# Performance work log

Measured on AMD Instinct MI355X. Metric: run time of the kernel, lower is better.

The kernel has to match this reference:

```python
import jax, jax.numpy as jnp
import numpy as np

NUM_EMBEDDINGS = 1024
EMBEDDING_DIM = 256


def setup_inputs() -> dict:
    key = jax.random.key(0)
    k1, k2 = jax.random.split(key)
    x = jax.random.normal(k1, (64, EMBEDDING_DIM, 32, 32), dtype=jnp.float32)
    # torch.nn.init.uniform_ default is U[0,1)
    embeddings = jax.random.uniform(k2, (EMBEDDING_DIM, NUM_EMBEDDINGS), dtype=jnp.float32)
    return {"x": x, "embeddings": embeddings}


def reference(x, embeddings):
    # x: [B, C, H, W] with C == embedding_dim; embeddings: [D, K]
    B, C, H, W = x.shape
    x_perm = jnp.transpose(x, (0, 2, 3, 1))           # [B, H, W, D]
    flat = x_perm.reshape(-1, C)                      # [N, D]
    sim = flat @ embeddings                           # [N, K] GEMM
    dists = (jnp.sum(flat * flat, axis=1, keepdims=True)
             + jnp.sum(embeddings * embeddings, axis=0)
             - 2.0 * sim)                             # [N, K]
    indices = jnp.argmin(dists, axis=1)               # [N]
    # one-hot @ embeddings.T is just a row gather of embeddings.T
    quantized = embeddings.T[indices]                 # [N, D]
    quantized = quantized.reshape(x_perm.shape)       # [B, H, W, D]
    # straight-through estimator
    q_ste = x_perm + jax.lax.stop_gradient(quantized - x_perm)
    q_ste = jnp.transpose(q_ste, (0, 3, 1, 2))        # [B, C, H, W]
    quantized = jnp.transpose(quantized, (0, 3, 1, 2))
    return q_ste, quantized, indices
```

## Files before the change

### kernel.cpp

```cpp
#include <hip/hip_runtime.h>

typedef unsigned short u16;
typedef unsigned int   u32;

#define DCH  256
#define KCB  1024
#define HW   1024
#define NPOS 65536
#define MARGIN 0.12f

#define ESQ_WS   0
#define IDX_WS   4096
#define FCNT_WS  266240
#define FLIST_WS 266304
#define ESQD_WS  528448ull
#define XH_WS    1048576ull
#define EH_WS    34603008ull

using f32x4 = __attribute__((ext_vector_type(4))) float;
using f16x8 = __attribute__((ext_vector_type(8))) _Float16;

__device__ __forceinline__ u16 f2h(float x) {
    _Float16 h = (_Float16)x;
    return *reinterpret_cast<u16*>(&h);
}
__device__ __forceinline__ u32 umin2(u32 a, u32 b) { return a < b ? a : b; }
__device__ __forceinline__ u32 umax2(u32 a, u32 b) { return a > b ? a : b; }

__device__ __forceinline__ void gl_lds16(const void* g, void* l) {
    __builtin_amdgcn_global_load_lds(
        (const __attribute__((address_space(1))) void*)g,
        (__attribute__((address_space(3))) void*)l, 16, 0, 0);
}

__device__ __forceinline__ void transpose_slice(const float* __restrict__ src,
                                                u16* __restrict__ dst,
                                                int b, int pc, int cc, int tid) {
    __shared__ float Xs[32][260];
    const int p0 = pc * 256;
    const int c0 = cc * 32;
    const size_t nbase = (size_t)b * 1024 + p0;
#pragma unroll
    for (int r = 0; r < 8; ++r) {
        int id4 = tid + 256 * r;
        int c = id4 >> 6;
        int q = id4 & 63;
        float4 v = *reinterpret_cast<const float4*>(
            src + (size_t)b * 262144 + (size_t)(c0 + c) * 1024 + p0 + q * 4);
        *reinterpret_cast<float4*>(&Xs[c][q * 4]) = v;
    }
    __syncthreads();
    const int p = tid;
#pragma unroll
    for (int dg = 0; dg < 4; ++dg) {
        u32 w0, w1, w2, w3;
        {
            float f0 = Xs[dg * 8 + 0][p], f1 = Xs[dg * 8 + 1][p];
            float f2 = Xs[dg * 8 + 2][p], f3 = Xs[dg * 8 + 3][p];
            float f4 = Xs[dg * 8 + 4][p], f5 = Xs[dg * 8 + 5][p];
            float f6 = Xs[dg * 8 + 6][p], f7 = Xs[dg * 8 + 7][p];
            w0 = (u32)f2h(f0) | ((u32)f2h(f1) << 16);
            w1 = (u32)f2h(f2) | ((u32)f2h(f3) << 16);
            w2 = (u32)f2h(f4) | ((u32)f2h(f5) << 16);
            w3 = (u32)f2h(f6) | ((u32)f2h(f7) << 16);
        }
        uint4 ov = {w0, w1, w2, w3};
        *reinterpret_cast<uint4*>(dst + (nbase + p) * 256 + c0 + dg * 8) = ov;
    }
}

__global__ __launch_bounds__(256) void prep_all(const float* __restrict__ X,
                                                const float* __restrict__ E,
                                                u16* __restrict__ Xh,
                                                u16* __restrict__ Eh,
                                                float* __restrict__ esq,
                                                double* __restrict__ esqd,
                                                int* __restrict__ fcnt) {
    const int tid = threadIdx.x;
    const int bid = blockIdx.x;
    if (bid < 2048) {
        transpose_slice(X, Xh, bid >> 5, (bid >> 3) & 3, bid & 7, tid);
    } else if (bid < 2080) {
        int b2 = bid - 2048;
        transpose_slice(E, Eh, 0, (b2 >> 3) & 3, b2 & 7, tid);
    } else {
        if (bid == 2080 && tid == 0) *fcnt = 0;
        int k = (bid - 2080) * 256 + tid;
        double s = 0.0;
#pragma unroll 8
        for (int c = 0; c < DCH; ++c) {
            double e = (double)E[c * KCB + k];
            s = fma(e, e, s);
        }
        esq[k] = (float)s;
        esqd[k] = s;
    }
}

#define BUFS  32768
#define EB_O  16384
#define ESQ_O 65536
#define MRG_O 69632
#define SM_SZ 72704

__global__ __launch_bounds__(256, 2) void vq_main_mfma(
        const u16* __restrict__ XhG, const u16* __restrict__ EhG,
        const float* __restrict__ esq,
        int* __restrict__ idx_out, int* __restrict__ flag_cnt,
        int* __restrict__ flag_list) {
    __shared__ alignas(16) char sm[SM_SZ];
    const int tid = threadIdx.x;
    const int l = tid & 63;
    const int w = tid >> 6;
    const int wm = w >> 1, wn = w & 1;
    const int pbase = blockIdx.x * 128;

    *reinterpret_cast<float4*>(sm + ESQ_O + tid * 16) =
        *reinterpret_cast<const float4*>(esq + tid * 4);

    const int srow = w * 32 + (l >> 3);
    const int sswz = ((l & 7) ^ (l >> 3)) * 16;
    const char* XhB = reinterpret_cast<const char*>(XhG);
    const char* EhB = reinterpret_cast<const char*>(EhG);
    const size_t xbase = (size_t)(pbase + srow) * 512 + sswz;
    const size_t ebase = (size_t)srow * 512 + sswz;

    const int sA0 = (((l >> 4) ^ (l & 7))) * 16;
    const int addrA0 = wm * 8192 + (l & 15) * 128 + sA0;
    const int addrB0 = wn * 8192 + (l & 15) * 128 + sA0;

    auto STAGE = [&](int bufo, int nt, int kt) {
        const size_t xo = xbase + (size_t)kt * 128;
        const size_t eo = ebase + (size_t)nt * 65536 + (size_t)kt * 128;
#pragma unroll
        for (int k = 0; k < 4; ++k) {
            gl_lds16(XhB + xo + k * 4096, sm + bufo + (w * 4 + k) * 1024);
            gl_lds16(EhB + eo + k * 4096, sm + bufo + EB_O + (w * 4 + k) * 1024);
        }
    };

    u32 b1[16], b2[16];
#pragma unroll
    for (int q = 0; q < 16; ++q) { b1[q] = 0xFFFFFFFFu; b2[q] = 0xFFFFFFFFu; }

    STAGE(0, 0, 0);
    __syncthreads();

    int step = 0;
    for (int nt = 0; nt < 8; ++nt) {
        f32x4 acc[4][4];
#pragma unroll
        for (int i = 0; i < 4; ++i)
#pragma unroll
            for (int j = 0; j < 4; ++j)
#pragma unroll
                for (int r = 0; r < 4; ++r) acc[i][j][r] = 0.f;

        for (int kt = 0; kt < 4; ++kt) {
            int nxt = step + 1;
            if (nxt < 32) STAGE((nxt & 1) * BUFS, nxt >> 2, nxt & 3);
            const char* bo = sm + (step & 1) * BUFS;
#pragma unroll
            for (int ds = 0; ds < 2; ++ds) {
                const int so = ds * 64;
                f16x8 a[4], bh[4];
#pragma unroll
                for (int i = 0; i < 4; ++i)
                    a[i] = *reinterpret_cast<const f16x8*>(bo + ((addrA0 ^ so) + i * 2048));
#pragma unroll
                for (int j = 0; j < 4; ++j)
                    bh[j] = *reinterpret_cast<const f16x8*>(bo + EB_O + ((addrB0 ^ so) + j * 2048));
#pragma unroll
                for (int i = 0; i < 4; ++i)
#pragma unroll
                    for (int j = 0; j < 4; ++j)
                        acc[i][j] = __builtin_amdgcn_mfma_f32_16x16x32_f16(a[i], bh[j], acc[i][j], 0, 0, 0);
            }
            __syncthreads();
            ++step;
        }

        const int kb = nt * 128 + wn * 64 + (l & 15);
        float eq[4];
#pragma unroll
        for (int j = 0; j < 4; ++j)
            eq[j] = *reinterpret_cast<const float*>(sm + ESQ_O + (kb + j * 16) * 4);
#pragma unroll
        for (int i = 0; i < 4; ++i)
#pragma unroll
            for (int j = 0; j < 4; ++j)
#pragma unroll
                for (int r = 0; r < 4; ++r) {
                    float s = fmaxf(fmaf(-2.f, acc[i][j][r], eq[j]), 0.f);
                    u32 v = (__float_as_uint(s) & 0xFFFFFC00u) | (u32)(kb + j * 16);
                    int ri = i * 4 + r;
                    u32 m1 = umin2(b1[ri], v);
                    b2[ri] = umin2(b2[ri], umax2(b1[ri], v));
                    b1[ri] = m1;
                }
    }

#pragma unroll
    for (int m = 1; m <= 8; m <<= 1) {
#pragma unroll
        for (int q = 0; q < 16; ++q) {
            u32 ob1 = (u32)__shfl_xor((int)b1[q], m);
            u32 ob2 = (u32)__shfl_xor((int)b2[q], m);
            u32 mx = umax2(b1[q], ob1);
            b1[q] = umin2(b1[q], ob1);
            b2[q] = umin2(umin2(b2[q], ob2), mx);
        }
    }

    if ((l & 15) == 0) {
#pragma unroll
        for (int i = 0; i < 4; ++i)
#pragma unroll
            for (int r = 0; r < 4; ++r) {
                int q = i * 4 + r;
                int rl = wm * 64 + i * 16 + (l >> 4) * 4 + r;
                *reinterpret_cast<u32*>(sm + MRG_O + (rl * 2 + wn) * 4) = b1[q];
                *reinterpret_cast<u32*>(sm + MRG_O + 1024 + (rl * 2 + wn) * 4) = b2[q];
            }
    }
    __syncthreads();
    if (tid < 128) {
        u32 a1 = *reinterpret_cast<u32*>(sm + MRG_O + (tid * 2 + 0) * 4);
        u32 a2 = *reinterpret_cast<u32*>(sm + MRG_O + 1024 + (tid * 2 + 0) * 4);
        u32 c1 = *reinterpret_cast<u32*>(sm + MRG_O + (tid * 2 + 1) * 4);
        u32 c2 = *reinterpret_cast<u32*>(sm + MRG_O + 1024 + (tid * 2 + 1) * 4);
        u32 P1 = umin2(a1, c1);
        u32 P2 = umin2(umin2(a2, c2), umax2(a1, c1));
        int n = pbase + tid;
        idx_out[n] = (int)(P1 & 1023u);
        float f1 = __uint_as_float(P1 & 0xFFFFFC00u);
        float f2 = __uint_as_float(P2 & 0xFFFFFC00u);
        if (f2 - f1 < MARGIN) {
            int s2 = atomicAdd(flag_cnt, 1);
            flag_list[s2] = n;
        }
    }
}

#define RFPB 4
__global__ __launch_bounds__(256) void vq_repair(const float* __restrict__ X,
                                                 const float* __restrict__ E,
                                                 const double* __restrict__ esqd,
                                                 int* __restrict__ idx_out,
                                                 const int* __restrict__ flag_cnt,
                                                 const int* __restrict__ flag_list) {
    __shared__ double xs[RFPB][256];
    __shared__ double rd[RFPB][256];
    __shared__ int    ri[RFPB][256];
    const int tid = threadIdx.x;
    const int cnt = *flag_cnt;
    for (int f0 = blockIdx.x * RFPB; f0 < cnt; f0 += gridDim.x * RFPB) {
#pragma unroll
        for (int g = 0; g < RFPB; ++g) {
            int f = f0 + g;
            int n = flag_list[f < cnt ? f : f0];
            int b = n >> 10, p = n & 1023;
            xs[g][tid] = (double)X[(size_t)b * 262144 + (size_t)tid * 1024 + p];
        }
        __syncthreads();
        double s[RFPB][4];
#pragma unroll
        for (int g = 0; g < RFPB; ++g)
#pragma unroll
            for (int j = 0; j < 4; ++j) s[g][j] = 0.0;
        const float4* Erow = reinterpret_cast<const float4*>(E) + tid;
#pragma unroll 2
        for (int c = 0; c < 256; ++c) {
            float4 ev = Erow[c * 256];
            double e0 = (double)ev.x, e1 = (double)ev.y, e2 = (double)ev.z, e3 = (double)ev.w;
#pragma unroll
            for (int g = 0; g < RFPB; ++g) {
                double xv = xs[g][c];
                s[g][0] = fma(xv, e0, s[g][0]);
                s[g][1] = fma(xv, e1, s[g][1]);
                s[g][2] = fma(xv, e2, s[g][2]);
                s[g][3] = fma(xv, e3, s[g][3]);
            }
        }
        const int k0 = tid * 4;
        const double eq0 = esqd[k0], eq1 = esqd[k0 + 1], eq2 = esqd[k0 + 2], eq3 = esqd[k0 + 3];
#pragma unroll
        for (int g = 0; g < RFPB; ++g) {
            double d0 = eq0 - 2.0 * s[g][0];
            double d1 = eq1 - 2.0 * s[g][1];
            double d2 = eq2 - 2.0 * s[g][2];
            double d3 = eq3 - 2.0 * s[g][3];
            double bd = d0; int bi = k0;
            if (d1 < bd) { bd = d1; bi = k0 + 1; }
            if (d2 < bd) { bd = d2; bi = k0 + 2; }
            if (d3 < bd) { bd = d3; bi = k0 + 3; }
            rd[g][tid] = bd; ri[g][tid] = bi;
        }
        __syncthreads();
        for (int off = 128; off > 0; off >>= 1) {
            if (tid < off) {
#pragma unroll
                for (int g = 0; g < RFPB; ++g) {
                    double od = rd[g][tid + off]; int oi = ri[g][tid + off];
                    if (od < rd[g][tid] || (od == rd[g][tid] && oi < ri[g][tid])) {
                        rd[g][tid] = od; ri[g][tid] = oi;
                    }
                }
            }
            __syncthreads();
        }
        if (tid < RFPB && (f0 + tid) < cnt) {
            idx_out[flag_list[f0 + tid]] = ri[tid][0];
        }
        __syncthreads();
    }
}

#define WCC 8
__global__ __launch_bounds__(256) void vq_write(const float* __restrict__ E,
                                                const int* __restrict__ idx_ws,
                                                float* __restrict__ out0,
                                                float* __restrict__ out1,
                                                float* __restrict__ out2) {
    __shared__ float Es[WCC][1024];
    const int tid = threadIdx.x;
    const int b   = blockIdx.x >> 5;
    const int cch = blockIdx.x & 31;
#pragma unroll
    for (int r = 0; r < 8; ++r) {
        int id4 = tid + 256 * r;
        int c = id4 >> 8;
        int q = id4 & 255;
        *reinterpret_cast<float4*>(&Es[c][q * 4]) =
            *reinterpret_cast<const float4*>(E + (size_t)(cch * WCC + c) * 1024 + q * 4);
    }
    int4 kv = *reinterpret_cast<const int4*>(idx_ws + b * 1024 + tid * 4);
    __syncthreads();
    if (cch == 0) {
        float4 v = {(float)kv.x, (float)kv.y, (float)kv.z, (float)kv.w};
        *reinterpret_cast<float4*>(out2 + b * 1024 + tid * 4) = v;
    }
#pragma unroll
    for (int c = 0; c < WCC; ++c) {
        float4 v = {Es[c][kv.x], Es[c][kv.y], Es[c][kv.z], Es[c][kv.w]};
        size_t o = (size_t)b * 262144 + (size_t)(cch * WCC + c) * 1024 + tid * 4;
        *reinterpret_cast<float4*>(out0 + o) = v;
        *reinterpret_cast<float4*>(out1 + o) = v;
    }
}

extern "C" void kernel_launch(void* const* d_in, const int* in_sizes, int n_in,
                              void* d_out, int out_size, void* d_ws, size_t ws_size,
                              hipStream_t stream) {
    const float* X = (const float*)d_in[0];
    const float* E = (const float*)d_in[1];
    float* out = (float*)d_out;
    char* ws = (char*)d_ws;

    float* esq   = (float*)(ws + ESQ_WS);
    int* idx     = (int*)(ws + IDX_WS);
    int* fcnt    = (int*)(ws + FCNT_WS);
    int* flist   = (int*)(ws + FLIST_WS);
    double* esqd = (double*)(ws + ESQD_WS);
    u16* Xh      = (u16*)(ws + XH_WS);
    u16* Eh      = (u16*)(ws + EH_WS);

    prep_all<<<2084, 256, 0, stream>>>(X, E, Xh, Eh, esq, esqd, fcnt);
    vq_main_mfma<<<512, 256, 0, stream>>>(Xh, Eh, esq, idx, fcnt, flist);
    vq_repair<<<1024, 256, 0, stream>>>(X, E, esqd, idx, fcnt, flist);
    vq_write<<<2048, 256, 0, stream>>>(E, idx,
                                       out,
                                       out + 16777216,
                                       out + 33554432);
}
```

Baseline: 162.8 us.

## Track top-2 distances as full floats with separate index, tighten repair margin

Replaces the packed uint key (mantissa-truncated distance with the code index in the low bits) with full-precision float best and second-best distances plus a separate argmin index. Because the distances are no longer quantized, the ambiguity margin for flagging rows for fp64 repair can shrink, so fewer rows go to the repair kernel. The repair kernel now handles fewer rows per block with twice the grid. In exchange the main loop carries more registers and extra select instructions, and the narrower margin relies on the fp16 GEMM error staying below it.

```diff
diff --git a/kernel.cpp b/kernel.cpp
--- a/kernel.cpp
+++ b/kernel.cpp
@@ -7,7 +7,7 @@
 #define KCB  1024
 #define HW   1024
 #define NPOS 65536
-#define MARGIN 0.12f
+#define MARGIN 0.07f
 
 #define ESQ_WS   0
 #define IDX_WS   4096
@@ -24,8 +24,6 @@
     _Float16 h = (_Float16)x;
     return *reinterpret_cast<u16*>(&h);
 }
-__device__ __forceinline__ u32 umin2(u32 a, u32 b) { return a < b ? a : b; }
-__device__ __forceinline__ u32 umax2(u32 a, u32 b) { return a > b ? a : b; }
 
 __device__ __forceinline__ void gl_lds16(const void* g, void* l) {
     __builtin_amdgcn_global_load_lds(
@@ -139,9 +137,10 @@
         }
     };
 
-    u32 b1[16], b2[16];
-#pragma unroll
-    for (int q = 0; q < 16; ++q) { b1[q] = 0xFFFFFFFFu; b2[q] = 0xFFFFFFFFu; }
+    float b1[16], b2[16];
+    int   i1[16];
+#pragma unroll
+    for (int q = 0; q < 16; ++q) { b1[q] = 3.4e38f; b2[q] = 3.4e38f; i1[q] = 0; }
 
     STAGE(0, 0, 0);
     __syncthreads();
@@ -191,12 +190,12 @@
             for (int j = 0; j < 4; ++j)
 #pragma unroll
                 for (int r = 0; r < 4; ++r) {
-                    float s = fmaxf(fmaf(-2.f, acc[i][j][r], eq[j]), 0.f);
-                    u32 v = (__float_as_uint(s) & 0xFFFFFC00u) | (u32)(kb + j * 16);
+                    float s = fmaf(-2.f, acc[i][j][r], eq[j]);
                     int ri = i * 4 + r;
-                    u32 m1 = umin2(b1[ri], v);
-                    b2[ri] = umin2(b2[ri], umax2(b1[ri], v));
-                    b1[ri] = m1;
+                    bool lt = s < b1[ri];
+                    b2[ri] = fminf(b2[ri], fmaxf(s, b1[ri]));
+                    i1[ri] = lt ? (kb + j * 16) : i1[ri];
+                    b1[ri] = fminf(b1[ri], s);
                 }
     }
 
@@ -204,11 +203,13 @@
     for (int m = 1; m <= 8; m <<= 1) {
 #pragma unroll
         for (int q = 0; q < 16; ++q) {
-            u32 ob1 = (u32)__shfl_xor((int)b1[q], m);
-            u32 ob2 = (u32)__shfl_xor((int)b2[q], m);
-            u32 mx = umax2(b1[q], ob1);
-            b1[q] = umin2(b1[q], ob1);
-            b2[q] = umin2(umin2(b2[q], ob2), mx);
+            float ob1 = __shfl_xor(b1[q], m);
+            float ob2 = __shfl_xor(b2[q], m);
+            int   oi  = __shfl_xor(i1[q], m);
+            bool lt = ob1 < b1[q];
+            b2[q] = fminf(fminf(b2[q], ob2), fmaxf(b1[q], ob1));
+            i1[q] = lt ? oi : i1[q];
+            b1[q] = fminf(b1[q], ob1);
         }
     }
 
@@ -219,30 +220,33 @@
             for (int r = 0; r < 4; ++r) {
                 int q = i * 4 + r;
                 int rl = wm * 64 + i * 16 + (l >> 4) * 4 + r;
-                *reinterpret_cast<u32*>(sm + MRG_O + (rl * 2 + wn) * 4) = b1[q];
-                *reinterpret_cast<u32*>(sm + MRG_O + 1024 + (rl * 2 + wn) * 4) = b2[q];
+                *reinterpret_cast<float*>(sm + MRG_O + (rl * 2 + wn) * 4) = b1[q];
+                *reinterpret_cast<float*>(sm + MRG_O + 1024 + (rl * 2 + wn) * 4) = b2[q];
+                *reinterpret_cast<int*>(sm + MRG_O + 2048 + (rl * 2 + wn) * 4) = i1[q];
             }
     }
     __syncthreads();
     if (tid < 128) {
-        u32 a1 = *reinterpret_cast<u32*>(sm + MRG_O + (tid * 2 + 0) * 4);
-        u32 a2 = *reinterpret_cast<u32*>(sm + MRG_O + 1024 + (tid * 2 + 0) * 4);
-        u32 c1 = *reinterpret_cast<u32*>(sm + MRG_O + (tid * 2 + 1) * 4);
-        u32 c2 = *reinterpret_cast<u32*>(sm + MRG_O + 1024 + (tid * 2 + 1) * 4);
-        u32 P1 = umin2(a1, c1);
-        u32 P2 = umin2(umin2(a2, c2), umax2(a1, c1));
+        float a1 = *reinterpret_cast<float*>(sm + MRG_O + (tid * 2 + 0) * 4);
+        float a2 = *reinterpret_cast<float*>(sm + MRG_O + 1024 + (tid * 2 + 0) * 4);
+        int   ai = *reinterpret_cast<int*>(sm + MRG_O + 2048 + (tid * 2 + 0) * 4);
+        float c1 = *reinterpret_cast<float*>(sm + MRG_O + (tid * 2 + 1) * 4);
+        float c2 = *reinterpret_cast<float*>(sm + MRG_O + 1024 + (tid * 2 + 1) * 4);
+        int   ci = *reinterpret_cast<int*>(sm + MRG_O + 2048 + (tid * 2 + 1) * 4);
+        bool lt = c1 < a1;
+        float B1 = fminf(a1, c1);
+        float B2 = fminf(fminf(a2, c2), fmaxf(a1, c1));
+        int I1 = lt ? ci : ai;
         int n = pbase + tid;
-        idx_out[n] = (int)(P1 & 1023u);
-        float f1 = __uint_as_float(P1 & 0xFFFFFC00u);
-        float f2 = __uint_as_float(P2 & 0xFFFFFC00u);
-        if (f2 - f1 < MARGIN) {
+        idx_out[n] = I1;
+        if (B2 - B1 < MARGIN) {
             int s2 = atomicAdd(flag_cnt, 1);
             flag_list[s2] = n;
         }
     }
 }
 
-#define RFPB 4
+#define RFPB 2
 __global__ __launch_bounds__(256) void vq_repair(const float* __restrict__ X,
                                                  const float* __restrict__ E,
                                                  const double* __restrict__ esqd,
@@ -367,7 +371,7 @@
 
     prep_all<<<2084, 256, 0, stream>>>(X, E, Xh, Eh, esq, esqd, fcnt);
     vq_main_mfma<<<512, 256, 0, stream>>>(Xh, Eh, esq, idx, fcnt, flist);
-    vq_repair<<<1024, 256, 0, stream>>>(X, E, esqd, idx, fcnt, flist);
+    vq_repair<<<2048, 256, 0, stream>>>(X, E, esqd, idx, fcnt, flist);
     vq_write<<<2048, 256, 0, stream>>>(E, idx,
                                        out,
                                        out + 16777216,
```

After: 151.4 us (median of 2 runs). 7.0% less time.
